# Kernel tuning notes

Measured on AMD Instinct MI355X. Metric: run time of the kernel, lower is better.

Reference implementation:

```python
import jax, jax.numpy as jnp
import numpy as np
from jax import lax

B, S, D, N_ORIG, GROUP_DIM, R = 8, 4096, 512, 4096, 64, 1024
EPS_MERGE = 1e-8
EPS_NORM = 1e-12  # F.normalize eps


def setup_inputs() -> dict:
    key = jax.random.key(0)
    k1, k2, k3 = jax.random.split(key, 3)
    x = jax.random.normal(k1, (B, S, D), dtype=jnp.float32)
    source = jax.random.normal(k2, (B, S, N_ORIG), dtype=jnp.float32)
    position_ids = jnp.arange(B * S, dtype=jnp.int32).reshape(B, S)
    # nn.Linear(dim, group_dim, bias=False) weight: (group_dim, dim)
    W = jax.random.normal(k3, (GROUP_DIM, D), dtype=jnp.float32) / np.sqrt(D)
    return {"x": x, "source": source, "position_ids": position_ids, "W": W, "r": R}


def _greedy_select(sim, r):
    """Greedy disjoint adjacent-pair selection; returns bool (S-1,) edge mask."""
    Sm1 = sim.shape[0]
    order = jnp.argsort(-sim, stable=True)  # matches torch.argsort(-sim, stable=True)

    def step(carry, p):
        used, sel, cnt = carry
        ok = (~used[p]) & (~used[p + 1]) & (cnt < r)
        used = used.at[p].set(used[p] | ok)
        used = used.at[p + 1].set(used[p + 1] | ok)
        sel = sel.at[p].set(ok)
        return (used, sel, cnt + ok.astype(jnp.int32)), None

    init = (jnp.zeros(Sm1 + 1, dtype=bool), jnp.zeros(Sm1, dtype=bool), jnp.int32(0))
    (_, sel, _), _ = lax.scan(step, init, order)
    return sel


def _merge_one(x, src, pos, sim, norms, r):
    Sl = x.shape[0]
    sel = _greedy_select(sim, r)  # sel[p] True => merge pair (p, p+1)
    w = norms[:, None]
    # weighted merge of adjacent pairs, written at position i = p
    merged = (w[:-1] * x[:-1] + w[1:] * x[1:]) / (w[:-1] + w[1:] + EPS_MERGE)
    x_out = jnp.concatenate([jnp.where(sel[:, None], merged, x[:-1]), x[-1:]], axis=0)
    src_out = src.at[:-1].add(jnp.where(sel[:, None], src[1:], 0.0))
    drop = jnp.concatenate([jnp.zeros(1, dtype=bool), sel])  # token p+1 dropped
    idx = jnp.arange(Sl)
    keep_order = jnp.argsort(jnp.where(drop, Sl + idx, idx))[: Sl - r]  # kept, in order
    return x_out[keep_order], src_out[keep_order], pos[keep_order]


def reference(x, source, position_ids, W, r):
    g = jnp.einsum("bsd,gd->bsg", x, W)  # group projection
    gnorms = jnp.linalg.norm(g, axis=-1)  # (B, S)
    g_unit = g / jnp.maximum(gnorms[..., None], EPS_NORM)
    sim = jnp.sum(g_unit[:, :-1] * g_unit[:, 1:], axis=-1)  # (B, S-1)
    merge = lambda xb, sb, pb, simb, nb: _merge_one(xb, sb, pb, simb, nb, r)
    return jax.vmap(merge)(x, source, position_ids, sim, gnorms)
```

## Files before the change

kernel.cpp:

```cpp
#include <hip/hip_runtime.h>
#include <hip/hip_bf16.h>
#include <stdint.h>

#define B_ 8
#define S_ 4096
#define D_ 512
#define G_ 64
#define R_ 1024
#define NO_ 4096
#define SO_ 3072
#define EPS_MERGE 1e-8f
#define EPS_NORM 1e-12f

#define WS_G     0ull
#define WS_GN    8388608ull
#define WS_KEYS  8519680ull
#define WS_KEPT  8781824ull

__global__ __launch_bounds__(256) void k1_proj(const float* __restrict__ x,
                                               const float* __restrict__ W,
                                               float* __restrict__ g,
                                               float* __restrict__ gn) {
  __shared__ float xs[32][132];
  __shared__ float wc[32][68];
  const int tid = threadIdx.x;
  const int gt  = tid & 15;
  const int rt  = tid >> 4;
  const int rb  = blockIdx.x * 128;
  const int g0  = gt * 4;
  const int r0  = rt * 8;
  float acc[8][4];
#pragma unroll
  for (int r = 0; r < 8; ++r)
#pragma unroll
    for (int j = 0; j < 4; ++j) acc[r][j] = 0.f;

  for (int kc = 0; kc < 16; ++kc) {
    const int kbase = kc * 32;
    __syncthreads();
#pragma unroll
    for (int i = 0; i < 4; ++i) {
      int f4i = tid + i * 256;
      int row_l = f4i >> 3;
      int kq = f4i & 7;
      const float4 v = *reinterpret_cast<const float4*>(
          &x[(size_t)(rb + row_l) * D_ + kbase + kq * 4]);
      xs[kq * 4 + 0][row_l] = v.x;
      xs[kq * 4 + 1][row_l] = v.y;
      xs[kq * 4 + 2][row_l] = v.z;
      xs[kq * 4 + 3][row_l] = v.w;
    }
#pragma unroll
    for (int i = 0; i < 2; ++i) {
      int f4i = tid + i * 256;
      int gg = f4i >> 3;
      int kq = f4i & 7;
      const float4 v = *reinterpret_cast<const float4*>(
          &W[(size_t)gg * D_ + kbase + kq * 4]);
      wc[kq * 4 + 0][gg] = v.x;
      wc[kq * 4 + 1][gg] = v.y;
      wc[kq * 4 + 2][gg] = v.z;
      wc[kq * 4 + 3][gg] = v.w;
    }
    __syncthreads();
#pragma unroll
    for (int k = 0; k < 32; ++k) {
      const float4 wv = *reinterpret_cast<const float4*>(&wc[k][g0]);
      const float4 xa = *reinterpret_cast<const float4*>(&xs[k][r0]);
      const float4 xb = *reinterpret_cast<const float4*>(&xs[k][r0 + 4]);
      const float xr[8] = {xa.x, xa.y, xa.z, xa.w, xb.x, xb.y, xb.z, xb.w};
#pragma unroll
      for (int r = 0; r < 8; ++r) {
        acc[r][0] = fmaf(xr[r], wv.x, acc[r][0]);
        acc[r][1] = fmaf(xr[r], wv.y, acc[r][1]);
        acc[r][2] = fmaf(xr[r], wv.z, acc[r][2]);
        acc[r][3] = fmaf(xr[r], wv.w, acc[r][3]);
      }
    }
  }
#pragma unroll
  for (int r = 0; r < 8; ++r) {
    const int row = rb + r0 + r;
    float4 v;
    v.x = acc[r][0]; v.y = acc[r][1]; v.z = acc[r][2]; v.w = acc[r][3];
    *reinterpret_cast<float4*>(&g[(size_t)row * G_ + g0]) = v;
    float ss = v.x * v.x + v.y * v.y + v.z * v.z + v.w * v.w;
    ss += __shfl_xor(ss, 1);
    ss += __shfl_xor(ss, 2);
    ss += __shfl_xor(ss, 4);
    ss += __shfl_xor(ss, 8);
    if (gt == 0) gn[row] = sqrtf(ss);
  }
}

__global__ __launch_bounds__(256) void k2_sim(const float* __restrict__ g,
                                              const float* __restrict__ gn,
                                              unsigned long long* __restrict__ prio) {
  const int wid = blockIdx.x * 4 + (threadIdx.x >> 6);
  const int lane = threadIdx.x & 63;
  if (wid >= B_ * (S_ - 1)) return;
  const int b = wid / (S_ - 1);
  const int e = wid - b * (S_ - 1);
  const size_t row = (size_t)b * S_ + e;
  const float a = g[row * G_ + lane];
  const float c = g[(row + 1) * G_ + lane];
  float p = a * c;
  p += __shfl_xor(p, 1);
  p += __shfl_xor(p, 2);
  p += __shfl_xor(p, 4);
  p += __shfl_xor(p, 8);
  p += __shfl_xor(p, 16);
  p += __shfl_xor(p, 32);
  if (lane == 0) {
    const float n0 = fmaxf(gn[row], EPS_NORM);
    const float n1 = fmaxf(gn[row + 1], EPS_NORM);
    const float sim = p / (n0 * n1);
    const unsigned int u = __float_as_uint(sim);
    const unsigned int m = (u & 0x80000000u) ? ~u : (u | 0x80000000u);
    prio[(size_t)b * S_ + e] =
        ((unsigned long long)m << 32) | (unsigned long long)(unsigned int)(4095 - e);
  }
}

__global__ __launch_bounds__(1024) void k3_match(const unsigned long long* __restrict__ prio,
                                                 unsigned int* __restrict__ kept) {
  __shared__ unsigned long long pr[4096];
  __shared__ unsigned char st[4096];
  __shared__ int hist[256];
  __shared__ int wsum[16];
  __shared__ int sh_undec;
  __shared__ int sh_need;
  __shared__ unsigned long long sh_prefix;

  const int tid = threadIdx.x;
  const int b = blockIdx.x;

  for (int i = tid; i < 4096; i += 1024) {
    pr[i] = (i < 4095) ? prio[(size_t)b * S_ + i] : 0ull;
    st[i] = (i < 4095) ? (unsigned char)0 : (unsigned char)2;
  }
  if (tid == 0) { sh_need = R_; sh_prefix = 0ull; }

  for (;;) {
    __syncthreads();
    if (tid == 0) sh_undec = 0;
    __syncthreads();
    bool any = false;
#pragma unroll
    for (int q = 0; q < 4; ++q) {
      const int e = (tid << 2) + q;
      if (e >= 4095) continue;
      if (st[e] != 0) continue;
      const unsigned char sl = e ? st[e - 1] : (unsigned char)2;
      const unsigned char sr = st[e + 1];
      if (sl == 1 || sr == 1) { st[e] = 2; continue; }
      const bool lok = (sl == 2) || (pr[e] > pr[e - 1]);
      const bool rok = (sr == 2) || (pr[e] > pr[e + 1]);
      if (lok && rok) st[e] = 1; else any = true;
    }
    if (any) sh_undec = 1;
    __syncthreads();
    if (sh_undec == 0) break;
  }

#pragma unroll 1
  for (int level = 0; level < 8; ++level) {
    const int shift = 56 - 8 * level;
    __syncthreads();
    if (tid < 256) hist[tid] = 0;
    __syncthreads();
    const unsigned long long pref = sh_prefix;
#pragma unroll
    for (int q = 0; q < 4; ++q) {
      const int e = (tid << 2) + q;
      if (e >= 4095) continue;
      if (st[e] != 1) continue;
      const unsigned long long p = pr[e];
      const bool match = (level == 0) || ((p >> (shift + 8)) == (pref >> (shift + 8)));
      if (match) atomicAdd(&hist[(int)((p >> shift) & 255ull)], 1);
    }
    __syncthreads();
    if (tid < 64) {
      const int lane = tid;
      const int h0 = hist[lane * 4 + 0], h1 = hist[lane * 4 + 1];
      const int h2 = hist[lane * 4 + 2], h3 = hist[lane * 4 + 3];
      const int gsum = h0 + h1 + h2 + h3;
      int s = gsum;
#pragma unroll
      for (int off = 1; off < 64; off <<= 1) {
        const int v = __shfl_down(s, off);
        if (lane + off < 64) s += v;
      }
      const int need = sh_need;
      const int suffAbove = s - gsum;
      if (suffAbove < need && s >= need) {
        const int hh[4] = {h0, h1, h2, h3};
        int cum = suffAbove;
        for (int q = 3; q >= 0; --q) {
          cum += hh[q];
          if (cum >= need) {
            sh_prefix = pref | ((unsigned long long)(lane * 4 + q) << shift);
            sh_need = need - (cum - hh[q]);
            break;
          }
        }
      }
    }
    __syncthreads();
  }
  const unsigned long long thresh = sh_prefix;
  __syncthreads();

  int c = 0;
  bool kp[4];
  const int s0 = tid * 4;
#pragma unroll
  for (int q = 0; q < 4; ++q) {
    const int s = s0 + q;
    const bool dropsel = (s > 0) && (st[s - 1] == 1) && (pr[s - 1] >= thresh);
    kp[q] = !dropsel;
    c += kp[q] ? 1 : 0;
  }
  const int lane = tid & 63, w = tid >> 6;
  int v = c;
#pragma unroll
  for (int off = 1; off < 64; off <<= 1) {
    const int t2 = __shfl_up(v, off);
    if (lane >= off) v += t2;
  }
  if (lane == 63) wsum[w] = v;
  __syncthreads();
  if (tid == 0) {
    int run = 0;
    for (int q = 0; q < 16; ++q) { const int t3 = wsum[q]; wsum[q] = run; run += t3; }
  }
  __syncthreads();
  int pos = (v - c) + wsum[w];
#pragma unroll
  for (int q = 0; q < 4; ++q) {
    if (kp[q]) {
      const int s = s0 + q;
      const unsigned int m =
          (s < 4095 && st[s] == 1 && pr[s] >= thresh) ? 0x80000000u : 0u;
      kept[b * SO_ + pos] = (unsigned int)s | m;
      ++pos;
    }
  }
}

__global__ __launch_bounds__(128) void k4_x(const float* __restrict__ x,
                                            const float* __restrict__ gn,
                                            const int* __restrict__ posid,
                                            const unsigned int* __restrict__ kept,
                                            float* __restrict__ outx,
                                            float* __restrict__ outpos) {
  const int blk = blockIdx.x;
  const int b = blk / SO_;
  const int j = blk - b * SO_;
  const unsigned int ent = kept[b * SO_ + j];
  const int s = (int)(ent & 0x7FFFFFFFu);
  const bool m = (ent & 0x80000000u) != 0u;
  const size_t rin = (size_t)b * S_ + s;
  const size_t rout = (size_t)b * SO_ + j;
  const int t = threadIdx.x;
  if (t == 0) outpos[rout] = (float)posid[rin];
  float4 a = *reinterpret_cast<const float4*>(&x[rin * D_ + t * 4]);
  float4 o;
  if (m) {
    const float w0 = gn[rin], w1 = gn[rin + 1];
    const float4 c2 = *reinterpret_cast<const float4*>(&x[(rin + 1) * D_ + t * 4]);
    const float den = w0 + w1 + EPS_MERGE;
    o.x = (w0 * a.x + w1 * c2.x) / den;
    o.y = (w0 * a.y + w1 * c2.y) / den;
    o.z = (w0 * a.z + w1 * c2.z) / den;
    o.w = (w0 * a.w + w1 * c2.w) / den;
  } else {
    o = a;
  }
  *reinterpret_cast<float4*>(&outx[rout * D_ + t * 4]) = o;
}

__global__ __launch_bounds__(256) void k5_src(const float* __restrict__ src,
                                              const unsigned int* __restrict__ kept,
                                              float* __restrict__ outs) {
  const int blk = blockIdx.x;
  const int b = blk / SO_;
  const int j = blk - b * SO_;
  const unsigned int ent = kept[b * SO_ + j];
  const int s = (int)(ent & 0x7FFFFFFFu);
  const bool m = (ent & 0x80000000u) != 0u;
  const size_t rin = ((size_t)b * S_ + s) * NO_;
  const size_t rout = ((size_t)b * SO_ + j) * NO_;
  const int t = threadIdx.x;
#pragma unroll
  for (int it = 0; it < 4; ++it) {
    const int f4 = t + it * 256;
    float4 a = *reinterpret_cast<const float4*>(&src[rin + (size_t)f4 * 4]);
    if (m) {
      const float4 c2 =
          *reinterpret_cast<const float4*>(&src[rin + NO_ + (size_t)f4 * 4]);
      a.x += c2.x; a.y += c2.y; a.z += c2.z; a.w += c2.w;
    }
    *reinterpret_cast<float4*>(&outs[rout + (size_t)f4 * 4]) = a;
  }
}

extern "C" void kernel_launch(void* const* d_in, const int* in_sizes, int n_in,
                              void* d_out, int out_size, void* d_ws, size_t ws_size,
                              hipStream_t stream) {
  (void)in_sizes; (void)n_in; (void)out_size; (void)ws_size;
  const float* x = (const float*)d_in[0];
  const float* src = (const float*)d_in[1];
  const int* posid = (const int*)d_in[2];
  const float* W = (const float*)d_in[3];

  char* ws = (char*)d_ws;
  float* g = (float*)(ws + WS_G);
  float* gn = (float*)(ws + WS_GN);
  unsigned long long* prio = (unsigned long long*)(ws + WS_KEYS);
  unsigned int* kept = (unsigned int*)(ws + WS_KEPT);

  float* outx = (float*)d_out;
  float* outs = outx + (size_t)B_ * SO_ * D_;
  float* outpos = outs + (size_t)B_ * SO_ * NO_;

  hipLaunchKernelGGL(k1_proj, dim3(256), dim3(256), 0, stream, x, W, g, gn);
  hipLaunchKernelGGL(k2_sim, dim3((B_ * (S_ - 1) + 3) / 4), dim3(256), 0, stream, g, gn, prio);
  hipLaunchKernelGGL(k3_match, dim3(B_), dim3(1024), 0, stream, prio, kept);
  hipLaunchKernelGGL(k4_x, dim3(B_ * SO_), dim3(128), 0, stream, x, gn, posid, kept,
                     outx, outpos);
  hipLaunchKernelGGL(k5_src, dim3(B_ * SO_), dim3(256), 0, stream, src, kept, outs);
}
```

Measured before the change: 272.7 us.

## Bit-pack matching state and resolve local rounds in registers in k3_match

```diff
diff --git a/kernel.cpp b/kernel.cpp
--- a/kernel.cpp
+++ b/kernel.cpp
@@ -122,59 +122,87 @@
   }
 }
 
-__global__ __launch_bounds__(1024) void k3_match(const unsigned long long* __restrict__ prio,
-                                                 unsigned int* __restrict__ kept) {
+__global__ __launch_bounds__(256) void k3_match(const unsigned long long* __restrict__ prio,
+                                                unsigned int* __restrict__ kept) {
   __shared__ unsigned long long pr[4096];
-  __shared__ unsigned char st[4096];
+  __shared__ unsigned int stw[258];
   __shared__ int hist[256];
-  __shared__ int wsum[16];
-  __shared__ int sh_undec;
+  __shared__ int wsum[4];
+  __shared__ int sh_flag;
   __shared__ int sh_need;
   __shared__ unsigned long long sh_prefix;
 
   const int tid = threadIdx.x;
   const int b = blockIdx.x;
 
-  for (int i = tid; i < 4096; i += 1024) {
-    pr[i] = (i < 4095) ? prio[(size_t)b * S_ + i] : 0ull;
-    st[i] = (i < 4095) ? (unsigned char)0 : (unsigned char)2;
-  }
-  if (tid == 0) { sh_need = R_; sh_prefix = 0ull; }
+#pragma unroll
+  for (int j = 0; j < 16; ++j) {
+    const int e = tid + j * 256;
+    pr[e] = (e < 4095) ? prio[(size_t)b * S_ + e] : 0ull;
+  }
+  if (tid == 0) {
+    stw[0] = 0xAAAAAAAAu;
+    stw[257] = 0xAAAAAAAAu;
+    sh_flag = 0; sh_need = R_; sh_prefix = 0ull;
+  }
+  stw[1 + tid] = (tid == 255) ? 0x80000000u : 0u;
+  __syncthreads();
+
+  unsigned int cl = 0, cr = 0;
+#pragma unroll
+  for (int j = 0; j < 16; ++j) {
+    const int e = tid * 16 + j;
+    const unsigned long long pe = pr[e];
+    const bool L = (e == 0) || (pe > pr[e - 1]);
+    const bool R = (e >= 4094) || (pe > pr[e + 1]);
+    cl |= (L ? 1u : 0u) << (2 * j);
+    cr |= (R ? 1u : 0u) << (2 * j);
+  }
 
   for (;;) {
     __syncthreads();
-    if (tid == 0) sh_undec = 0;
-    __syncthreads();
-    bool any = false;
-#pragma unroll
-    for (int q = 0; q < 4; ++q) {
-      const int e = (tid << 2) + q;
-      if (e >= 4095) continue;
-      if (st[e] != 0) continue;
-      const unsigned char sl = e ? st[e - 1] : (unsigned char)2;
-      const unsigned char sr = st[e + 1];
-      if (sl == 1 || sr == 1) { st[e] = 2; continue; }
-      const bool lok = (sl == 2) || (pr[e] > pr[e - 1]);
-      const bool rok = (sr == 2) || (pr[e] > pr[e + 1]);
-      if (lok && rok) st[e] = 1; else any = true;
-    }
-    if (any) sh_undec = 1;
-    __syncthreads();
-    if (sh_undec == 0) break;
-  }
+    if (tid == 0) sh_flag = 0;
+    __syncthreads();
+    unsigned int u = stw[1 + tid];
+    const unsigned int lw = stw[tid];
+    const unsigned int rw = stw[2 + tid];
+    const unsigned int linb = (lw >> 30) & 1u;
+    const unsigned int loutb = (lw >> 31) & 1u;
+    const unsigned int rinb = (rw & 1u) << 30;
+    const unsigned int routb = ((rw >> 1) & 1u) << 30;
+    bool changed = false;
+    for (;;) {
+      const unsigned int a = u & 0x55555555u;
+      const unsigned int d = (u >> 1) & 0x55555555u;
+      const unsigned int lin = (a << 2) | linb;
+      const unsigned int lout = (d << 2) | loutb;
+      const unsigned int rin = (a >> 2) | rinb;
+      const unsigned int rout = (d >> 2) | routb;
+      const unsigned int undec = ~(a | d) & 0x55555555u;
+      const unsigned int nout = undec & (lin | rin);
+      const unsigned int nin = undec & ~lin & ~rin & (lout | cl) & (rout | cr);
+      if (!(nin | nout)) break;
+      u |= nin | (nout << 1);
+      changed = true;
+    }
+    if (changed) { stw[1 + tid] = u; sh_flag = 1; }
+    __syncthreads();
+    if (sh_flag == 0) break;
+  }
+
+  const unsigned int inw = stw[1 + tid] & 0x55555555u;
 
 #pragma unroll 1
   for (int level = 0; level < 8; ++level) {
     const int shift = 56 - 8 * level;
     __syncthreads();
-    if (tid < 256) hist[tid] = 0;
+    hist[tid] = 0;
     __syncthreads();
     const unsigned long long pref = sh_prefix;
 #pragma unroll
-    for (int q = 0; q < 4; ++q) {
-      const int e = (tid << 2) + q;
-      if (e >= 4095) continue;
-      if (st[e] != 1) continue;
+    for (int j = 0; j < 16; ++j) {
+      if (!((inw >> (2 * j)) & 1u)) continue;
+      const int e = tid * 16 + j;
       const unsigned long long p = pr[e];
       const bool match = (level == 0) || ((p >> (shift + 8)) == (pref >> (shift + 8)));
       if (match) atomicAdd(&hist[(int)((p >> shift) & 255ull)], 1);
@@ -182,6 +210,7 @@
     __syncthreads();
     if (tid < 64) {
       const int lane = tid;
+      const int need = sh_need;
       const int h0 = hist[lane * 4 + 0], h1 = hist[lane * 4 + 1];
       const int h2 = hist[lane * 4 + 2], h3 = hist[lane * 4 + 3];
       const int gsum = h0 + h1 + h2 + h3;
@@ -191,7 +220,6 @@
         const int v = __shfl_down(s, off);
         if (lane + off < 64) s += v;
       }
-      const int need = sh_need;
       const int suffAbove = s - gsum;
       if (suffAbove < need && s >= need) {
         const int hh[4] = {h0, h1, h2, h3};
@@ -209,17 +237,20 @@
     __syncthreads();
   }
   const unsigned long long thresh = sh_prefix;
-  __syncthreads();
+  const unsigned int previnw = stw[tid] & 0x55555555u;
 
   int c = 0;
-  bool kp[4];
-  const int s0 = tid * 4;
-#pragma unroll
-  for (int q = 0; q < 4; ++q) {
-    const int s = s0 + q;
-    const bool dropsel = (s > 0) && (st[s - 1] == 1) && (pr[s - 1] >= thresh);
-    kp[q] = !dropsel;
-    c += kp[q] ? 1 : 0;
+  unsigned int kpbits = 0;
+#pragma unroll
+  for (int j = 0; j < 16; ++j) {
+    const int s = tid * 16 + j;
+    bool selprev = false;
+    if (s > 0) {
+      const unsigned int ib =
+          (j == 0) ? ((previnw >> 30) & 1u) : ((inw >> (2 * (j - 1))) & 1u);
+      selprev = ib && (pr[s - 1] >= thresh);
+    }
+    if (!selprev) { kpbits |= 1u << j; ++c; }
   }
   const int lane = tid & 63, w = tid >> 6;
   int v = c;
@@ -232,16 +263,16 @@
   __syncthreads();
   if (tid == 0) {
     int run = 0;
-    for (int q = 0; q < 16; ++q) { const int t3 = wsum[q]; wsum[q] = run; run += t3; }
+    for (int q = 0; q < 4; ++q) { const int t3 = wsum[q]; wsum[q] = run; run += t3; }
   }
   __syncthreads();
   int pos = (v - c) + wsum[w];
 #pragma unroll
-  for (int q = 0; q < 4; ++q) {
-    if (kp[q]) {
-      const int s = s0 + q;
+  for (int j = 0; j < 16; ++j) {
+    if ((kpbits >> j) & 1u) {
+      const int s = tid * 16 + j;
       const unsigned int m =
-          (s < 4095 && st[s] == 1 && pr[s] >= thresh) ? 0x80000000u : 0u;
+          (((inw >> (2 * j)) & 1u) && pr[s] >= thresh) ? 0x80000000u : 0u;
       kept[b * SO_ + pos] = (unsigned int)s | m;
       ++pos;
     }
@@ -326,7 +357,7 @@
 
   hipLaunchKernelGGL(k1_proj, dim3(256), dim3(256), 0, stream, x, W, g, gn);
   hipLaunchKernelGGL(k2_sim, dim3((B_ * (S_ - 1) + 3) / 4), dim3(256), 0, stream, g, gn, prio);
-  hipLaunchKernelGGL(k3_match, dim3(B_), dim3(1024), 0, stream, prio, kept);
+  hipLaunchKernelGGL(k3_match, dim3(B_), dim3(256), 0, stream, prio, kept);
   hipLaunchKernelGGL(k4_x, dim3(B_ * SO_), dim3(128), 0, stream, x, gn, posid, kept,
                      outx, outpos);
   hipLaunchKernelGGL(k5_src, dim3(B_ * SO_), dim3(256), 0, stream, src, kept, outs);
```

New measurement: 277.3 us. No clear change (+1.7%).
